# Performance work log

Hardware: AMD Instinct MI355X
Metric: run time of the kernel (lower is better)

Reference implementation:

```python
import jax, jax.numpy as jnp
import numpy as np

B, NV, HID, TDIM = 1024, 256, 256, 128
NODE_IN = 2 + 4 + TDIM  # coords + pos_enc(4) + time_emb


def _sinusoidal_pos_emb(t, dim):
    # standard SinusoidalPosEmb: cat(sin, cos) of t * exp(-i*log(1e4)/(half-1))
    half = dim // 2
    freqs = jnp.exp(-np.log(10000.0) * jnp.arange(half, dtype=t.dtype) / (half - 1))
    ang = t[:, None] * freqs[None, :]
    return jnp.concatenate([jnp.sin(ang), jnp.cos(ang)], axis=-1)  # [B, dim]


def setup_inputs() -> dict:
    key = jax.random.key(0)
    ks = jax.random.split(key, 10)
    s = lambda fan_in: 1.0 / np.sqrt(fan_in)
    return {
        "x": jax.random.normal(ks[0], (B, NV * 2), dtype=jnp.float32),
        "t": jax.random.uniform(ks[1], (B,), dtype=jnp.float32) * 1000.0,
        "time_w": jax.random.normal(ks[2], (TDIM, TDIM), dtype=jnp.float32) * s(TDIM),
        "time_b": jnp.zeros((TDIM,), dtype=jnp.float32),
        "W0": jax.random.normal(ks[3], (NODE_IN, HID), dtype=jnp.float32) * s(NODE_IN),
        "b0": jnp.zeros((HID,), dtype=jnp.float32),
        "W1": jax.random.normal(ks[4], (HID, HID), dtype=jnp.float32) * s(HID),
        "b1": jnp.zeros((HID,), dtype=jnp.float32),
        "W2": jax.random.normal(ks[5], (HID, HID), dtype=jnp.float32) * s(HID),
        "b2": jnp.zeros((HID,), dtype=jnp.float32),
    }


def reference(x, t, time_w, time_b, W0, b0, W1, b1, W2, b2):
    Bsz, D = x.shape
    n = D // 2
    coords = x.reshape(Bsz, n, 2)  # [B, n, 2]

    # cycle positional features (pos_enc_dim=4): sin/cos of vertex angle + 2nd harmonic
    pos = jnp.arange(n, dtype=x.dtype)
    theta = (2.0 * jnp.pi) * pos / n
    pe = jnp.stack([jnp.sin(theta), jnp.cos(theta), jnp.sin(2.0 * theta), jnp.cos(2.0 * theta)], axis=-1)
    pe = jnp.broadcast_to(pe[None], (Bsz, n, 4))

    # time MLP: SinusoidalPosEmb -> Linear -> SiLU, broadcast to every node of the graph
    temb = jax.nn.silu(_sinusoidal_pos_emb(t, time_w.shape[0]) @ time_w + time_b)  # [B, TDIM]
    temb = jnp.broadcast_to(temb[:, None, :], (Bsz, n, temb.shape[-1]))

    h = jnp.concatenate([coords, pe, temb], axis=-1)  # [B, n, NODE_IN]

    # GCN layers over cycle adjacency with self-loops, symmetric-normalized (deg=3 -> 1/3).
    # Cycle structure: neighbors are prev/next vertex within each polygon -> jnp.roll on axis 1.
    for W, b in ((W0, b0), (W1, b1), (W2, b2)):
        s = h @ W + b  # support = x W + b
        agg = (s + jnp.roll(s, 1, axis=1) + jnp.roll(s, -1, axis=1)) / 3.0
        h = jax.nn.silu(agg)

    # mean pooling per graph (scatter_mean over graph_index == mean over vertex axis here)
    return h.mean(axis=1)  # [B, HID]
```

## Files before the change

kernel.cpp:

```cpp
#include <hip/hip_runtime.h>
#include <cstdint>

typedef __attribute__((ext_vector_type(8)))  short bf16x8;
typedef __attribute__((ext_vector_type(16))) float f32x16;
typedef __attribute__((ext_vector_type(2)))  float f32x2;
typedef __attribute__((ext_vector_type(4)))  int   i32x4;

__device__ __forceinline__ unsigned short f2bf(float x) {
  unsigned u = __float_as_uint(x);
  u += 0x7fffu + ((u >> 16) & 1u);
  return (unsigned short)(u >> 16);
}
__device__ __forceinline__ float bf2f(unsigned short h) {
  return __uint_as_float(((unsigned)h) << 16);
}
__device__ __forceinline__ float silu_f(float v) {
  return v * __builtin_amdgcn_rcpf(1.0f + __expf(-v));
}
__device__ __forceinline__ unsigned pk2bf(float lo, float hi) {
#if defined(__has_builtin)
#if __has_builtin(__builtin_amdgcn_cvt_pk_bf16_f32)
  auto v = __builtin_amdgcn_cvt_pk_bf16_f32(lo, hi);
  unsigned u; __builtin_memcpy(&u, &v, 4); return u;
#else
  return ((unsigned)f2bf(hi) << 16) | (unsigned)f2bf(lo);
#endif
#else
  return ((unsigned)f2bf(hi) << 16) | (unsigned)f2bf(lo);
#endif
}
__device__ __forceinline__ unsigned lo_pack(unsigned x, unsigned y) {
  return __builtin_amdgcn_perm(y, x, 0x05040100u);
}
__device__ __forceinline__ unsigned hi_pack(unsigned x, unsigned y) {
  return __builtin_amdgcn_perm(y, x, 0x07060302u);
}
__device__ __forceinline__ void gl_lds16(const unsigned short* g, unsigned short* l) {
  __builtin_amdgcn_global_load_lds(
      (const __attribute__((address_space(1))) unsigned int*)g,
      (__attribute__((address_space(3))) unsigned int*)l, 16, 0, 0);
}
__device__ __forceinline__ void stage(const unsigned short* src, unsigned short* lds_w,
                                      const int tid, const int w, const int chunks) {
  for (int it = 0; it * 512 < chunks; ++it) {
    const int ci = it * 512 + tid;
    if (ci < chunks)
      gl_lds16(src + ci * 8, lds_w + (it * 512 + w * 64) * 8);
  }
}

__global__ void pack_kernel(const float* __restrict__ W0, const float* __restrict__ W1,
                            const float* __restrict__ W2,
                            unsigned short* __restrict__ packW) {
  __shared__ float ldsF[16][257];
  const int s = blockIdx.x, tid = threadIdx.x;
  const float* W; int KT, kmax, base, kt;
  if (s < 9)       { W = W0; KT = 9;  kmax = 134; base = 0;      kt = s; }
  else if (s < 25) { W = W1; KT = 16; kmax = 256; base = 36864;  kt = s - 9; }
  else             { W = W2; KT = 16; kmax = 256; base = 102400; kt = s - 25; }
  const int k0 = kt * 16;
#pragma unroll
  for (int i = 0; i < 8; ++i) {
    const int idx = i * 512 + tid;
    const int kl = idx >> 8, col = idx & 255;
    const int kg = k0 + kl;
    ldsF[kl][col] = (kg < kmax) ? W[kg * 256 + col] : 0.0f;
  }
  __syncthreads();
  const int g = tid >> 7, t = (tid >> 6) & 1, lane = tid & 63;
  const int col = g * 64 + t * 32 + (lane & 31);
  const int kb = 8 * (lane >> 5);
  unsigned u0 = pk2bf(ldsF[kb + 0][col], ldsF[kb + 1][col]);
  unsigned u1 = pk2bf(ldsF[kb + 2][col], ldsF[kb + 3][col]);
  unsigned u2 = pk2bf(ldsF[kb + 4][col], ldsF[kb + 5][col]);
  unsigned u3 = pk2bf(ldsF[kb + 6][col], ldsF[kb + 7][col]);
  unsigned short* dst = packW + base + g * (KT * 1024) + t * (KT * 512) + kt * 512 + lane * 8;
  i32x4 v = { (int)u0, (int)u1, (int)u2, (int)u3 };
  *(i32x4*)dst = v;
}

template <int KT, int LAYER>
__device__ __forceinline__ void gcn_layer(
    const int tid, const int w, const int lane, const int q, const int c, const int sig,
    const unsigned short* __restrict__ packL,
    const unsigned short* __restrict__ nextL, const int nextChunks,
    const float* __restrict__ BIAS,
    const bf16x8* Aold, bf16x8* Anew,
    unsigned short* wbuf, unsigned short* bnd,
    unsigned int* scr3_w, float* poolw) {
#pragma unroll
  for (int g = 0; g < 4; ++g) {
    if (g < 3)           stage(packL + (g + 1) * (KT * 1024), wbuf + ((g + 1) & 1) * 8192,
                               tid, w, KT * 64);
    else if (nextChunks) stage(nextL, wbuf + ((g + 1) & 1) * 8192, tid, w, nextChunks);

    const unsigned short* srcg = packL + g * (KT * 1024);
    f32x16 acc0, acc1;
#pragma unroll
    for (int i = 0; i < 16; ++i) { acc0[i] = 0.f; acc1[i] = 0.f; }
    {
      const bf16x8* wb0 = (const bf16x8*)(wbuf + (g & 1) * 8192);
      const bf16x8* wb1 = (const bf16x8*)(srcg + KT * 512);
#pragma unroll
      for (int kt = 0; kt < KT; ++kt) {
        bf16x8 b0 = wb0[kt * 64 + lane];
        bf16x8 b1 = wb1[kt * 64 + lane];
        acc0 = __builtin_amdgcn_mfma_f32_32x32x16_bf16(Aold[kt], b0, acc0, 0, 0, 0);
        acc1 = __builtin_amdgcn_mfma_f32_32x32x16_bf16(Aold[kt], b1, acc1, 0, 0, 0);
      }
    }

    unsigned short* bndp = bnd + (g & 1) * 2048;
    if (q == 0) { bndp[(w * 2 + 0) * 64 + c]      = f2bf(acc0[0]);
                  bndp[(w * 2 + 0) * 64 + 32 + c] = f2bf(acc1[0]); }
    else        { bndp[(w * 2 + 1) * 64 + c]      = f2bf(acc0[15]);
                  bndp[(w * 2 + 1) * 64 + 32 + c] = f2bf(acc1[15]); }
    __syncthreads();

    const float e0t0  = __shfl_xor(acc0[0], 32);
    const float e0t1  = __shfl_xor(acc1[0], 32);
    const float e15t0 = __shfl_xor(acc0[15], 32);
    const float e15t1 = __shfl_xor(acc1[15], 32);
    const float bp0 = bf2f(bndp[(((w + 7) & 7) * 2 + 1) * 64 + c]);
    const float bp1 = bf2f(bndp[(((w + 7) & 7) * 2 + 1) * 64 + 32 + c]);
    const float bn0 = bf2f(bndp[(((w + 1) & 7) * 2 + 0) * 64 + c]);
    const float bn1 = bf2f(bndp[(((w + 1) & 7) * 2 + 0) * 64 + 32 + c]);
    const float bias0 = BIAS[g * 64 + c], bias1 = BIAS[g * 64 + 32 + c];
    const float T = 0.33333333333f;
    float ps0 = 0.f, ps1 = 0.f;
#pragma unroll
    for (int r = 0; r < 16; ++r) {
      float pr0, pr1, nx0, nx1;
      if (r > 0)       { pr0 = acc0[r - 1]; pr1 = acc1[r - 1]; }
      else             { pr0 = q ? e15t0 : bp0; pr1 = q ? e15t1 : bp1; }
      if (r < 15)      { nx0 = acc0[r + 1]; nx1 = acc1[r + 1]; }
      else             { nx0 = q ? bn0 : e0t0; nx1 = q ? bn1 : e0t1; }
      f32x2 v2;
      v2.x = (pr0 + acc0[r] + nx0) * T + bias0;
      v2.y = (pr1 + acc1[r] + nx1) * T + bias1;
      f32x2 ex; ex.x = __expf(-v2.x); ex.y = __expf(-v2.y);
      f32x2 den = ex + 1.0f;
      f32x2 y2;
      y2.x = v2.x * __builtin_amdgcn_rcpf(den.x);
      y2.y = v2.y * __builtin_amdgcn_rcpf(den.y);
      if constexpr (LAYER == 2) { ps0 += y2.x; ps1 += y2.y; }
      else {
        scr3_w[(16 * q + r) * 34 + c] = pk2bf(y2.x, y2.y);
      }
    }

    if constexpr (LAYER == 2) {
      ps0 += __shfl_xor(ps0, 32);
      ps1 += __shfl_xor(ps1, 32);
      if (q == 0) { poolw[w * 256 + g * 64 + c]      = ps0;
                    poolw[w * 256 + g * 64 + 32 + c] = ps1; }
    } else {
      const unsigned int* sb = scr3_w + sig * 34;
      uint2 d0 = *(const uint2*)(sb + 8 * q + 0);
      uint2 d1 = *(const uint2*)(sb + 8 * q + 2);
      uint2 d2 = *(const uint2*)(sb + 8 * q + 4);
      uint2 d3 = *(const uint2*)(sb + 8 * q + 6);
      uint2 e0 = *(const uint2*)(sb + 16 + 8 * q + 0);
      uint2 e1 = *(const uint2*)(sb + 16 + 8 * q + 2);
      uint2 e2 = *(const uint2*)(sb + 16 + 8 * q + 4);
      uint2 e3 = *(const uint2*)(sb + 16 + 8 * q + 6);
      i32x4 f0 = { (int)lo_pack(d0.x, d0.y), (int)lo_pack(d1.x, d1.y),
                   (int)lo_pack(d2.x, d2.y), (int)lo_pack(d3.x, d3.y) };
      i32x4 f1 = { (int)lo_pack(e0.x, e0.y), (int)lo_pack(e1.x, e1.y),
                   (int)lo_pack(e2.x, e2.y), (int)lo_pack(e3.x, e3.y) };
      i32x4 f2v = { (int)hi_pack(d0.x, d0.y), (int)hi_pack(d1.x, d1.y),
                    (int)hi_pack(d2.x, d2.y), (int)hi_pack(d3.x, d3.y) };
      i32x4 f3 = { (int)hi_pack(e0.x, e0.y), (int)hi_pack(e1.x, e1.y),
                   (int)hi_pack(e2.x, e2.y), (int)hi_pack(e3.x, e3.y) };
      Anew[g * 4 + 0] = __builtin_bit_cast(bf16x8, f0);
      Anew[g * 4 + 1] = __builtin_bit_cast(bf16x8, f1);
      Anew[g * 4 + 2] = __builtin_bit_cast(bf16x8, f2v);
      Anew[g * 4 + 3] = __builtin_bit_cast(bf16x8, f3);
    }
  }
}

__global__ __launch_bounds__(512, 2) void poly_kernel(
    const float* __restrict__ x, const float* __restrict__ t,
    const float* __restrict__ tw, const float* __restrict__ tb,
    const unsigned short* __restrict__ packW,
    const float* __restrict__ B0, const float* __restrict__ B1,
    const float* __restrict__ B2, float* __restrict__ out) {
  __shared__ __align__(16) unsigned short wbuf[2 * 8192];
  __shared__ __align__(16) unsigned short bnd[4096];
  __shared__ __align__(16) unsigned int   scr3[8 * 1088];
  __shared__ __align__(16) unsigned short temb_sh[160];

  const int tid = threadIdx.x;
  const int w = tid >> 6, lane = tid & 63;
  const int q = lane >> 5, c = lane & 31;
  const int b = blockIdx.x;
  const int sig = (c & 3) + 4 * ((c >> 3) & 3) + 16 * ((c >> 2) & 1);

  stage(packW, wbuf, tid, w, 9 * 64);

  {
    float* e_sh = (float*)bnd;
    float* part = (float*)scr3;
    if (tid < 128) {
      const float tv = t[b];
      const int i = tid & 63;
      const float f = expf(-0.14619588396823767f * (float)i);
      const float ang = tv * f;
      e_sh[tid] = (tid < 64) ? sinf(ang) : cosf(ang);
    }
    __syncthreads();
    {
      const int j = tid & 127, p = tid >> 7;
      float a = 0.f;
#pragma unroll 8
      for (int kk = 0; kk < 32; ++kk) {
        const int k = p * 32 + kk;
        a += e_sh[k] * tw[k * 128 + j];
      }
      part[tid] = a;
    }
    __syncthreads();
    if (tid < 128) {
      const float a = tb[tid] + part[tid] + part[128 + tid] + part[256 + tid] + part[384 + tid];
      temb_sh[6 + tid] = f2bf(silu_f(a));
      if (tid < 6)  temb_sh[tid] = 0;
      if (tid < 10) temb_sh[134 + tid] = 0;
    }
    __syncthreads();
  }

  bf16x8 A0[9], A1[16], A2[16];
  {
#pragma unroll
    for (int kt = 0; kt < 9; ++kt)
      A0[kt] = *(const bf16x8*)(temb_sh + kt * 16 + q * 8);
    if (q == 0) {
      const int n = w * 32 + sig;
      const float2 xy = ((const float2*)x)[b * 256 + n];
      const float th = 0.024543692605870074f * (float)n;
      A0[0][0] = (short)f2bf(xy.x);
      A0[0][1] = (short)f2bf(xy.y);
      A0[0][2] = (short)f2bf(sinf(th));
      A0[0][3] = (short)f2bf(cosf(th));
      A0[0][4] = (short)f2bf(sinf(2.f * th));
      A0[0][5] = (short)f2bf(cosf(2.f * th));
    }
  }

  unsigned int* scr3_w = scr3 + w * 1088;
  float* poolw = (float*)scr3;
  gcn_layer< 9, 0>(tid, w, lane, q, c, sig, packW,          packW + 36864,  16 * 64,
                   B0, A0, A1, wbuf, bnd, scr3_w, poolw);
  gcn_layer<16, 1>(tid, w, lane, q, c, sig, packW + 36864,  packW + 102400, 16 * 64,
                   B1, A1, A2, wbuf, bnd, scr3_w, poolw);
  gcn_layer<16, 2>(tid, w, lane, q, c, sig, packW + 102400, nullptr,        0,
                   B2, A2, A1, wbuf, bnd, scr3_w, poolw);

  __syncthreads();
  if (tid < 256) {
    float s = 0.f;
#pragma unroll
    for (int ww = 0; ww < 8; ++ww) s += poolw[ww * 256 + tid];
    out[b * 256 + tid] = s * (1.f / 256.f);
  }
}

extern "C" void kernel_launch(void* const* d_in, const int* in_sizes, int n_in,
                              void* d_out, int out_size, void* d_ws, size_t ws_size,
                              hipStream_t stream) {
  const float* x  = (const float*)d_in[0];
  const float* t  = (const float*)d_in[1];
  const float* tw = (const float*)d_in[2];
  const float* tb = (const float*)d_in[3];
  const float* W0 = (const float*)d_in[4];
  const float* b0 = (const float*)d_in[5];
  const float* W1 = (const float*)d_in[6];
  const float* b1 = (const float*)d_in[7];
  const float* W2 = (const float*)d_in[8];
  const float* b2 = (const float*)d_in[9];

  unsigned short* packW = (unsigned short*)d_ws;
  float* out = (float*)d_out;

  pack_kernel<<<41, 512, 0, stream>>>(W0, W1, W2, packW);
  poly_kernel<<<1024, 512, 0, stream>>>(x, t, tw, tb, packW, b0, b1, b2, out);
}
```

Before: 214.0 us.

## Replace block barriers with per-wave neighbor flags and read weights from global

```diff
diff --git a/kernel.cpp b/kernel.cpp
--- a/kernel.cpp
+++ b/kernel.cpp
@@ -35,19 +35,6 @@
 __device__ __forceinline__ unsigned hi_pack(unsigned x, unsigned y) {
   return __builtin_amdgcn_perm(y, x, 0x07060302u);
 }
-__device__ __forceinline__ void gl_lds16(const unsigned short* g, unsigned short* l) {
-  __builtin_amdgcn_global_load_lds(
-      (const __attribute__((address_space(1))) unsigned int*)g,
-      (__attribute__((address_space(3))) unsigned int*)l, 16, 0, 0);
-}
-__device__ __forceinline__ void stage(const unsigned short* src, unsigned short* lds_w,
-                                      const int tid, const int w, const int chunks) {
-  for (int it = 0; it * 512 < chunks; ++it) {
-    const int ci = it * 512 + tid;
-    if (ci < chunks)
-      gl_lds16(src + ci * 8, lds_w + (it * 512 + w * 64) * 8);
-  }
-}
 
 __global__ void pack_kernel(const float* __restrict__ W0, const float* __restrict__ W1,
                             const float* __restrict__ W2,
@@ -81,25 +68,23 @@
 
 template <int KT, int LAYER>
 __device__ __forceinline__ void gcn_layer(
-    const int tid, const int w, const int lane, const int q, const int c, const int sig,
+    const int w, const int lane, const int q, const int c, const int sig,
+    const int wp, const int wn, const int ebase,
     const unsigned short* __restrict__ packL,
-    const unsigned short* __restrict__ nextL, const int nextChunks,
     const float* __restrict__ BIAS,
     const bf16x8* Aold, bf16x8* Anew,
-    unsigned short* wbuf, unsigned short* bnd,
+    unsigned short* bndE, unsigned int* flagsL,
     unsigned int* scr3_w, float* poolw) {
 #pragma unroll
   for (int g = 0; g < 4; ++g) {
-    if (g < 3)           stage(packL + (g + 1) * (KT * 1024), wbuf + ((g + 1) & 1) * 8192,
-                               tid, w, KT * 64);
-    else if (nextChunks) stage(nextL, wbuf + ((g + 1) & 1) * 8192, tid, w, nextChunks);
-
+    const int e = ebase + g;
     const unsigned short* srcg = packL + g * (KT * 1024);
+
     f32x16 acc0, acc1;
 #pragma unroll
     for (int i = 0; i < 16; ++i) { acc0[i] = 0.f; acc1[i] = 0.f; }
     {
-      const bf16x8* wb0 = (const bf16x8*)(wbuf + (g & 1) * 8192);
+      const bf16x8* wb0 = (const bf16x8*)srcg;
       const bf16x8* wb1 = (const bf16x8*)(srcg + KT * 512);
 #pragma unroll
       for (int kt = 0; kt < KT; ++kt) {
@@ -110,21 +95,33 @@
       }
     }
 
-    unsigned short* bndp = bnd + (g & 1) * 2048;
-    if (q == 0) { bndp[(w * 2 + 0) * 64 + c]      = f2bf(acc0[0]);
-                  bndp[(w * 2 + 0) * 64 + 32 + c] = f2bf(acc1[0]); }
-    else        { bndp[(w * 2 + 1) * 64 + c]      = f2bf(acc0[15]);
-                  bndp[(w * 2 + 1) * 64 + 32 + c] = f2bf(acc1[15]); }
-    __syncthreads();
+    {
+      unsigned short* myb = bndE + (e * 8 + w) * 128;
+      if (q == 0) { myb[c]      = f2bf(acc0[0]);  myb[32 + c] = f2bf(acc1[0]);  }
+      else        { myb[64 + c] = f2bf(acc0[15]); myb[96 + c] = f2bf(acc1[15]); }
+      if (lane == 0)
+        __hip_atomic_store(&flagsL[e * 8 + w], 1u, __ATOMIC_RELEASE,
+                           __HIP_MEMORY_SCOPE_WORKGROUP);
+    }
 
     const float e0t0  = __shfl_xor(acc0[0], 32);
     const float e0t1  = __shfl_xor(acc1[0], 32);
     const float e15t0 = __shfl_xor(acc0[15], 32);
     const float e15t1 = __shfl_xor(acc1[15], 32);
-    const float bp0 = bf2f(bndp[(((w + 7) & 7) * 2 + 1) * 64 + c]);
-    const float bp1 = bf2f(bndp[(((w + 7) & 7) * 2 + 1) * 64 + 32 + c]);
-    const float bn0 = bf2f(bndp[(((w + 1) & 7) * 2 + 0) * 64 + c]);
-    const float bn1 = bf2f(bndp[(((w + 1) & 7) * 2 + 0) * 64 + 32 + c]);
+
+#pragma clang loop unroll(disable)
+    while (__hip_atomic_load(&flagsL[e * 8 + wp], __ATOMIC_ACQUIRE,
+                             __HIP_MEMORY_SCOPE_WORKGROUP) == 0u)
+      __builtin_amdgcn_s_sleep(1);
+#pragma clang loop unroll(disable)
+    while (__hip_atomic_load(&flagsL[e * 8 + wn], __ATOMIC_ACQUIRE,
+                             __HIP_MEMORY_SCOPE_WORKGROUP) == 0u)
+      __builtin_amdgcn_s_sleep(1);
+
+    const float bp0 = bf2f(bndE[(e * 8 + wp) * 128 + 64 + c]);
+    const float bp1 = bf2f(bndE[(e * 8 + wp) * 128 + 96 + c]);
+    const float bn0 = bf2f(bndE[(e * 8 + wn) * 128 + c]);
+    const float bn1 = bf2f(bndE[(e * 8 + wn) * 128 + 32 + c]);
     const float bias0 = BIAS[g * 64 + c], bias1 = BIAS[g * 64 + 32 + c];
     const float T = 0.33333333333f;
     float ps0 = 0.f, ps1 = 0.f;
@@ -186,21 +183,23 @@
     const unsigned short* __restrict__ packW,
     const float* __restrict__ B0, const float* __restrict__ B1,
     const float* __restrict__ B2, float* __restrict__ out) {
-  __shared__ __align__(16) unsigned short wbuf[2 * 8192];
-  __shared__ __align__(16) unsigned short bnd[4096];
+  __shared__ __align__(16) unsigned short bndE[12288];
+  __shared__ unsigned int flagsL[96];
   __shared__ __align__(16) unsigned int   scr3[8 * 1088];
+  __shared__ float poolL[2048];
   __shared__ __align__(16) unsigned short temb_sh[160];
 
   const int tid = threadIdx.x;
   const int w = tid >> 6, lane = tid & 63;
   const int q = lane >> 5, c = lane & 31;
+  const int wp = (w + 7) & 7, wn = (w + 1) & 7;
   const int b = blockIdx.x;
   const int sig = (c & 3) + 4 * ((c >> 3) & 3) + 16 * ((c >> 2) & 1);
 
-  stage(packW, wbuf, tid, w, 9 * 64);
+  if (lane < 12) flagsL[lane * 8 + w] = 0;
 
   {
-    float* e_sh = (float*)bnd;
+    float* e_sh = (float*)bndE;
     float* part = (float*)scr3;
     if (tid < 128) {
       const float tv = t[b];
@@ -249,19 +248,18 @@
   }
 
   unsigned int* scr3_w = scr3 + w * 1088;
-  float* poolw = (float*)scr3;
-  gcn_layer< 9, 0>(tid, w, lane, q, c, sig, packW,          packW + 36864,  16 * 64,
-                   B0, A0, A1, wbuf, bnd, scr3_w, poolw);
-  gcn_layer<16, 1>(tid, w, lane, q, c, sig, packW + 36864,  packW + 102400, 16 * 64,
-                   B1, A1, A2, wbuf, bnd, scr3_w, poolw);
-  gcn_layer<16, 2>(tid, w, lane, q, c, sig, packW + 102400, nullptr,        0,
-                   B2, A2, A1, wbuf, bnd, scr3_w, poolw);
+  gcn_layer< 9, 0>(w, lane, q, c, sig, wp, wn, 0, packW,          B0, A0, A1,
+                   bndE, flagsL, scr3_w, poolL);
+  gcn_layer<16, 1>(w, lane, q, c, sig, wp, wn, 4, packW + 36864,  B1, A1, A2,
+                   bndE, flagsL, scr3_w, poolL);
+  gcn_layer<16, 2>(w, lane, q, c, sig, wp, wn, 8, packW + 102400, B2, A2, A1,
+                   bndE, flagsL, scr3_w, poolL);
 
   __syncthreads();
   if (tid < 256) {
     float s = 0.f;
 #pragma unroll
-    for (int ww = 0; ww < 8; ++ww) s += poolw[ww * 256 + tid];
+    for (int ww = 0; ww < 8; ++ww) s += poolL[ww * 256 + tid];
     out[b * 256 + tid] = s * (1.f / 256.f);
   }
 }
```

New measurement: 211.1 us. Within noise of the previous version (-1.4%).
